# Performance work log

Measured on AMD Instinct MI355X. Metric: run time of the kernel, lower is better.

## Reference

```python
import jax, jax.numpy as jnp
import numpy as np

D = 256          # d_model
NH = 8           # heads
NP = 4           # points per level
NL = 4           # feature levels
DH = D // NH     # head dim = 32
MLP = 4 * D      # 1024
B = 2
SHAPES = [(128, 128), (64, 64), (32, 32), (16, 16)]
LQ = sum(h * w for h, w in SHAPES)  # 21760
EPS = 1e-6


def layer_norm(x, g, b):
    mu = jnp.mean(x, axis=-1, keepdims=True)
    var = jnp.mean(jnp.square(x - mu), axis=-1, keepdims=True)
    return (x - mu) * jax.lax.rsqrt(var + EPS) * g + b


def bilinear_sample(val_l, loc, Hs, Ws):
    # val_l: [B, Hs*Ws, NH, DH]; loc: [B, Lq, NH, NP, 2] normalized in [0,1]
    v = val_l.transpose(0, 2, 1, 3)                      # [B, NH, HW, DH]
    x = loc[..., 0] * Ws - 0.5                           # [B, Lq, NH, NP]
    y = loc[..., 1] * Hs - 0.5
    x0 = jnp.floor(x); y0 = jnp.floor(y)
    lx = x - x0; ly = y - y0
    x0i = x0.astype(jnp.int32); y0i = y0.astype(jnp.int32)

    def gather(xi, yi):
        inb = (xi >= 0) & (xi < Ws) & (yi >= 0) & (yi < Hs)
        idx = jnp.clip(yi, 0, Hs - 1) * Ws + jnp.clip(xi, 0, Ws - 1)
        idx = idx.transpose(0, 2, 1, 3)                  # [B, NH, Lq, NP]
        sh = idx.shape
        idxf = idx.reshape(sh[0], sh[1], -1)
        g = jax.vmap(jax.vmap(lambda vv, ii: vv[ii]))(v, idxf)
        g = g.reshape(sh[0], sh[1], sh[2], sh[3], v.shape[-1])
        return g * inb.transpose(0, 2, 1, 3)[..., None].astype(g.dtype)

    wt = lambda a: a.transpose(0, 2, 1, 3)[..., None]    # -> [B, NH, Lq, NP, 1]
    out = (gather(x0i, y0i) * wt((1 - lx) * (1 - ly))
           + gather(x0i + 1, y0i) * wt(lx * (1 - ly))
           + gather(x0i, y0i + 1) * wt((1 - lx) * ly)
           + gather(x0i + 1, y0i + 1) * wt(lx * ly))
    return out                                            # [B, NH, Lq, NP, DH]


def setup_inputs() -> dict:
    key = jax.random.key(0)
    ks = jax.random.split(key, 16)
    ss = np.array(SHAPES, dtype=np.int64)
    lsi = np.concatenate([[0], np.cumsum(ss[:, 0] * ss[:, 1])[:-1]]).astype(np.int64)
    s = 0.02
    return {
        'src': jax.random.normal(ks[0], (B, LQ, D), jnp.float32),
        'pos': jax.random.normal(ks[1], (B, LQ, D), jnp.float32),
        'reference_points': jax.random.uniform(ks[2], (B, LQ, NL, 2), jnp.float32),
        'spatial_shapes': ss,
        'level_start_index': lsi,
        'g1': jnp.ones((D,), jnp.float32), 'beta1': jnp.zeros((D,), jnp.float32),
        'w_off': jax.random.normal(ks[3], (D, NH * NL * NP * 2), jnp.float32) * 0.01,
        'b_off': jax.random.normal(ks[4], (NH * NL * NP * 2,), jnp.float32) * 0.1,
        'w_attn': jax.random.normal(ks[5], (D, NH * NL * NP), jnp.float32) * s,
        'b_attn': jnp.zeros((NH * NL * NP,), jnp.float32),
        'w_val': jax.random.normal(ks[6], (D, D), jnp.float32) * s,
        'b_val': jnp.zeros((D,), jnp.float32),
        'w_out': jax.random.normal(ks[7], (D, D), jnp.float32) * s,
        'b_out': jnp.zeros((D,), jnp.float32),
        'g2': jnp.ones((D,), jnp.float32), 'beta2': jnp.zeros((D,), jnp.float32),
        'w_fc1': jax.random.normal(ks[8], (D, MLP), jnp.float32) * s,
        'b_fc1': jnp.zeros((MLP,), jnp.float32),
        'w_fc2': jax.random.normal(ks[9], (MLP, D), jnp.float32) * s,
        'b_fc2': jnp.zeros((D,), jnp.float32),
    }


def reference(src, pos, reference_points, spatial_shapes, level_start_index,
              g1, beta1, w_off, b_off, w_attn, b_attn, w_val, b_val,
              w_out, b_out, g2, beta2, w_fc1, b_fc1, w_fc2, b_fc2):
    ss = np.asarray(spatial_shapes)
    lsi = np.asarray(level_start_index)
    Bsz, Lq, _ = src.shape

    # --- pre-norm + multi-scale deformable attention + residual ---
    x = layer_norm(src, g1, beta1)
    q = x + pos
    val = (x @ w_val + b_val).reshape(Bsz, Lq, NH, DH)
    off = (q @ w_off + b_off).reshape(Bsz, Lq, NH, NL, NP, 2)
    aw = jax.nn.softmax((q @ w_attn + b_attn).reshape(Bsz, Lq, NH, NL * NP), axis=-1)
    aw = aw.reshape(Bsz, Lq, NH, NL, NP)

    out = jnp.zeros((Bsz, Lq, NH, DH), src.dtype)
    for l in range(NL):
        Hs, Ws = int(ss[l, 0]), int(ss[l, 1])
        start = int(lsi[l])
        vl = val[:, start:start + Hs * Ws]                       # [B, HW, NH, DH]
        norm = jnp.array([Ws, Hs], src.dtype)
        loc = reference_points[:, :, None, l, None, :] + off[:, :, :, l] / norm
        samp = bilinear_sample(vl, loc, Hs, Ws)                  # [B, NH, Lq, NP, DH]
        a = aw[:, :, :, l].transpose(0, 2, 1, 3)                 # [B, NH, Lq, NP]
        out = out + jnp.einsum('bhqp,bhqpd->bqhd', a, samp)
    attn_out = out.reshape(Bsz, Lq, D) @ w_out + b_out
    src2 = src + attn_out

    # --- pre-norm MLP + residual ---
    y = layer_norm(src2, g2, beta2)
    ffn = jax.nn.relu(y @ w_fc1 + b_fc1) @ w_fc2 + b_fc2
    return src2 + ffn
```

## Files before the change

kernel.cpp:

```cpp
#include <hip/hip_runtime.h>

#define DMODEL 256
#define NHEAD 8
#define NPOINT 4
#define NLEVEL 4
#define DHEAD 32
#define MLPD 1024
#define BSZ 2
#define LQTOK 21760
#define NTOK (BSZ * LQTOK)
#define LNEPS 1e-6f

typedef __attribute__((ext_vector_type(8))) short short8;
typedef __attribute__((ext_vector_type(4))) float f32x4;
typedef __attribute__((ext_vector_type(2))) float f32x2;

__device__ __forceinline__ float bf2f(unsigned short u) {
  unsigned int i = ((unsigned int)u) << 16;
  return __builtin_bit_cast(float, i);
}
__device__ __forceinline__ unsigned short f2bf(float f) {
  unsigned int i = __builtin_bit_cast(unsigned int, f);
  i += 0x7fff + ((i >> 16) & 1);
  return (unsigned short)(i >> 16);
}
__device__ __forceinline__ float bflo(unsigned int u) {
  return __builtin_bit_cast(float, u << 16);
}
__device__ __forceinline__ float bfhi(unsigned int u) {
  return __builtin_bit_cast(float, u & 0xffff0000u);
}

__device__ __forceinline__ void pk_fma_blo(f32x2& d, f32x2 a, f32x2 b) {
  asm("v_pk_fma_f32 %0, %1, %2, %0 op_sel:[0,0,0] op_sel_hi:[1,0,1]"
      : "+v"(d)
      : "v"(a), "v"(b));
}
__device__ __forceinline__ void pk_fma_bhi(f32x2& d, f32x2 a, f32x2 b) {
  asm("v_pk_fma_f32 %0, %1, %2, %0 op_sel:[0,1,0] op_sel_hi:[1,1,1]"
      : "+v"(d)
      : "v"(a), "v"(b));
}

__device__ __forceinline__ void gload_lds16(const unsigned short* g,
                                            unsigned short* lds) {
  __builtin_amdgcn_global_load_lds(
      (const __attribute__((address_space(1))) unsigned int*)g,
      (__attribute__((address_space(3))) unsigned int*)lds, 16, 0, 0);
}

template <bool EMITQ>
__global__ __launch_bounds__(256) void ln_bf16(
    const float* __restrict__ in, const float* __restrict__ g,
    const float* __restrict__ beta, unsigned short* __restrict__ o,
    const float* __restrict__ pos, unsigned short* __restrict__ q) {
  const int w = threadIdx.x >> 6, lane = threadIdx.x & 63;
  const size_t t = (size_t)blockIdx.x * 4 + w;
  const size_t base = t * DMODEL + lane * 4;
  float4 v = *(const float4*)(in + base);
  float s = (v.x + v.y) + (v.z + v.w);
#pragma unroll
  for (int off = 32; off; off >>= 1) s += __shfl_xor(s, off, 64);
  float mu = s * (1.0f / DMODEL);
  float dx = v.x - mu, dy = v.y - mu, dz = v.z - mu, dw = v.w - mu;
  float s2 = (dx * dx + dy * dy) + (dz * dz + dw * dw);
#pragma unroll
  for (int off = 32; off; off >>= 1) s2 += __shfl_xor(s2, off, 64);
  float rs = rsqrtf(s2 * (1.0f / DMODEL) + LNEPS);
  float4 gg = *(const float4*)(g + lane * 4);
  float4 bb = *(const float4*)(beta + lane * 4);
  unsigned short r0 = f2bf(dx * rs * gg.x + bb.x);
  unsigned short r1 = f2bf(dy * rs * gg.y + bb.y);
  unsigned short r2 = f2bf(dz * rs * gg.z + bb.z);
  unsigned short r3 = f2bf(dw * rs * gg.w + bb.w);
  unsigned int lo = ((unsigned int)r1 << 16) | r0;
  unsigned int hi = ((unsigned int)r3 << 16) | r2;
  *(uint2*)(o + base) = make_uint2(lo, hi);
  if (EMITQ) {
    float4 p = *(const float4*)(pos + base);
    unsigned short q0 = f2bf(bf2f(r0) + p.x);
    unsigned short q1 = f2bf(bf2f(r1) + p.y);
    unsigned short q2 = f2bf(bf2f(r2) + p.z);
    unsigned short q3 = f2bf(bf2f(r3) + p.w);
    unsigned int ql = ((unsigned int)q1 << 16) | q0;
    unsigned int qh = ((unsigned int)q3 << 16) | q2;
    *(uint2*)(q + base) = make_uint2(ql, qh);
  }
}

__global__ __launch_bounds__(256) void transpose_bf16(const float* __restrict__ W,
                                                      unsigned short* __restrict__ Wt,
                                                      int K, int N) {
  __shared__ float tile[32][33];
  int k0 = blockIdx.x * 32, n0 = blockIdx.y * 32;
  int tx = threadIdx.x & 31, ty = threadIdx.x >> 5;
  for (int i = ty; i < 32; i += 8) tile[i][tx] = W[(size_t)(k0 + i) * N + n0 + tx];
  __syncthreads();
  for (int i = ty; i < 32; i += 8)
    Wt[(size_t)(n0 + i) * K + k0 + tx] = f2bf(tile[tx][i]);
}

template <int OMODE>
__global__ __launch_bounds__(256) void gemm_mfma(
    const unsigned short* __restrict__ A, const unsigned short* __restrict__ Wt,
    const float* __restrict__ bias, const float* __restrict__ res,
    void* __restrict__ Cout, void* __restrict__ Cout2, int M, int N, int K) {
  __shared__ __attribute__((aligned(16))) unsigned short As[128 * 32];
  __shared__ __attribute__((aligned(16))) unsigned short Bs[128 * 32];
  const int tid = threadIdx.x;
  const unsigned gx = gridDim.x, gy = gridDim.y;
  const unsigned nwg = gx * gy;
  const unsigned orig = blockIdx.y * gx + blockIdx.x;
  const unsigned xcd = orig & 7u, rest = orig >> 3;
  const unsigned qq = nwg >> 3, rr = nwg & 7u;
  const unsigned wgid =
      (xcd < rr ? xcd * (qq + 1) : rr * (qq + 1) + (xcd - rr) * qq) + rest;
  const int m0 = (int)(wgid / gy) * 128;
  const int n0 = (int)(wgid % gy) * 128;
  const int wave = tid >> 6, lane = tid & 63;
  const int wm = (wave & 1) * 64, wn = (wave >> 1) * 64;
  const int lr = lane & 15, quad = lane >> 4;
  f32x4 acc[4][4] = {};
  for (int k0 = 0; k0 < K; k0 += 32) {
    __syncthreads();
#pragma unroll
    for (int r = 0; r < 2; r++) {
      int c = r * 256 + tid;
      int row = c >> 2, col8 = (c & 3) * 8;
      gload_lds16(Wt + (size_t)(n0 + row) * K + k0 + col8,
                  &Bs[(r * 256 + wave * 64) * 8]);
    }
#pragma unroll
    for (int r = 0; r < 2; r++) {
      int c = r * 256 + tid;
      int row = c >> 2, col8 = (c & 3) * 8;
      gload_lds16(A + (size_t)(m0 + row) * K + k0 + col8,
                  &As[(r * 256 + wave * 64) * 8]);
    }
    __syncthreads();
    short8 af[4], bfr[4];
#pragma unroll
    for (int i = 0; i < 4; i++)
      af[i] = *(const short8*)(&As[(wm + i * 16 + lr) * 32 + quad * 8]);
#pragma unroll
    for (int j = 0; j < 4; j++)
      bfr[j] = *(const short8*)(&Bs[(wn + j * 16 + lr) * 32 + quad * 8]);
#pragma unroll
    for (int i = 0; i < 4; i++)
#pragma unroll
      for (int j = 0; j < 4; j++)
        acc[i][j] = __builtin_amdgcn_mfma_f32_16x16x32_bf16(af[i], bfr[j],
                                                            acc[i][j], 0, 0, 0);
  }
#pragma unroll
  for (int i = 0; i < 4; i++) {
    int rbase = m0 + wm + i * 16 + quad * 4;
#pragma unroll
    for (int j = 0; j < 4; j++) {
      int col = n0 + wn + j * 16 + lr;
      float bv = (OMODE == 4 && col >= 256) ? res[col - 256] : bias[col];
#pragma unroll
      for (int r = 0; r < 4; r++) {
        float v = acc[i][j][r] + bv;
        if (OMODE == 2) v = fmaxf(v, 0.0f);
        if (OMODE == 4) {
          size_t row = (size_t)(rbase + r);
          if (col < 256)
            ((unsigned short*)Cout)[row * 256 + col] = f2bf(v);
          else
            ((unsigned short*)Cout2)[row * 128 + (col - 256)] = f2bf(v);
        } else {
          size_t idx = (size_t)(rbase + r) * N + col;
          if (OMODE == 3) {
            ((float*)Cout)[idx] = v + res[idx];
          } else {
            ((unsigned short*)Cout)[idx] = f2bf(v);
          }
        }
      }
    }
  }
}

__global__ __launch_bounds__(256) void deform_sample(
    const unsigned short* __restrict__ val, const unsigned short* __restrict__ off,
    const unsigned short* __restrict__ logits, const float* __restrict__ refp,
    unsigned short* __restrict__ out) {
  __shared__ __attribute__((aligned(16))) int sIdx[4][16][8][4];
  __shared__ __attribute__((aligned(16))) float sW[4][16][8][4];
  const int w = threadIdx.x >> 6, lane = threadIdx.x & 63;
  const int bq = blockIdx.x * 4 + w;
  const int b = __builtin_amdgcn_readfirstlane(bq / LQTOK);
  {
    const int HW_[4] = {128, 64, 32, 16};
    const int LSI_[4] = {0, 16384, 20480, 21504};
    int u0 = 2 * lane;
    int h = u0 >> 4;
    int lvl = (u0 >> 2) & 3;
    int pt0 = u0 & 15;
    int HW = HW_[lvl];
    float2 rp = ((const float2*)refp)[(size_t)bq * 4 + lvl];
    uint2 ov = *(const uint2*)(off + (size_t)bq * 256 + 4 * lane);
    unsigned int lgu = *(const unsigned int*)(logits + (size_t)bq * 128 + 2 * lane);
    float lg0 = bflo(lgu), lg1 = bfhi(lgu);
    float mx = fmaxf(lg0, lg1);
#pragma unroll
    for (int s = 1; s < 8; s <<= 1) mx = fmaxf(mx, __shfl_xor(mx, s, 64));
    float e0 = expf(lg0 - mx), e1 = expf(lg1 - mx);
    float es = e0 + e1;
#pragma unroll
    for (int s = 1; s < 8; s <<= 1) es += __shfl_xor(es, s, 64);
    float inv = 1.0f / es;
    float a01[2] = {e0 * inv, e1 * inv};
    unsigned int ovv[2] = {ov.x, ov.y};
    int hb2 = h * (DHEAD * 2);
#pragma unroll
    for (int c = 0; c < 2; c++) {
      float x = fmaf(rp.x, (float)HW, bflo(ovv[c])) - 0.5f;
      float y = fmaf(rp.y, (float)HW, bfhi(ovv[c])) - 0.5f;
      float xf = floorf(x), yf = floorf(y);
      int x0 = (int)xf, y0 = (int)yf;
      float lx = x - xf, ly = y - yf;
      int x0c = min(max(x0, 0), HW - 1);
      int x1c = min(max(x0 + 1, 0), HW - 1);
      int y0c = min(max(y0, 0), HW - 1);
      int y1c = min(max(y0 + 1, 0), HW - 1);
      float m0x = (x0 >= 0 && x0 < HW) ? 1.f : 0.f;
      float m1x = (x0 + 1 >= 0 && x0 + 1 < HW) ? 1.f : 0.f;
      float m0y = (y0 >= 0 && y0 < HW) ? 1.f : 0.f;
      float m1y = (y0 + 1 >= 0 && y0 + 1 < HW) ? 1.f : 0.f;
      float a = a01[c];
      int pt = pt0 + c;
      int hs = h ^ (pt & 7);
      int r0 = (LSI_[lvl] + y0c * HW) * (DMODEL * 2) + hb2;
      int r1 = (LSI_[lvl] + y1c * HW) * (DMODEL * 2) + hb2;
      *(int4*)sIdx[w][pt][hs] =
          make_int4(r0 + x0c * (DMODEL * 2), r0 + x1c * (DMODEL * 2),
                    r1 + x0c * (DMODEL * 2), r1 + x1c * (DMODEL * 2));
      *(float4*)sW[w][pt][hs] =
          make_float4((1.f - lx) * (1.f - ly) * m0x * m0y * a,
                      lx * (1.f - ly) * m1x * m0y * a,
                      (1.f - lx) * ly * m0x * m1y * a,
                      lx * ly * m1x * m1y * a);
    }
  }
  __builtin_amdgcn_wave_barrier();
  const int h2 = lane >> 3, g = lane & 7;
  const char* basep =
      (const char*)val + (size_t)b * ((size_t)LQTOK * DMODEL * 2);
  const int goff = g * 8;
  f32x2 a01v = {0.f, 0.f}, a23v = {0.f, 0.f};
#pragma unroll
  for (int pb = 0; pb < 4; pb++) {
    int4 ix[4];
    f32x4 wt4[4];
#pragma unroll
    for (int p = 0; p < 4; p++) {
      int pt = pb * 4 + p;
      int hs = h2 ^ (pt & 7);
      ix[p] = *(const int4*)sIdx[w][pt][hs];
      wt4[p] = *(const f32x4*)sW[w][pt][hs];
    }
    uint2 v4[4][4];
#pragma unroll
    for (int p = 0; p < 4; p++) {
      v4[p][0] = *(const uint2*)(basep + (unsigned)(ix[p].x + goff));
      v4[p][1] = *(const uint2*)(basep + (unsigned)(ix[p].y + goff));
      v4[p][2] = *(const uint2*)(basep + (unsigned)(ix[p].z + goff));
      v4[p][3] = *(const uint2*)(basep + (unsigned)(ix[p].w + goff));
    }
#pragma unroll
    for (int p = 0; p < 4; p++) {
      f32x2 w01 = __builtin_shufflevector(wt4[p], wt4[p], 0, 1);
      f32x2 w23 = __builtin_shufflevector(wt4[p], wt4[p], 2, 3);
#pragma unroll
      for (int k = 0; k < 4; k++) {
        uint2 u = v4[p][k];
        f32x2 vlo, vhi;
        vlo[0] = bflo(u.x);
        vlo[1] = bfhi(u.x);
        vhi[0] = bflo(u.y);
        vhi[1] = bfhi(u.y);
        f32x2 wp = (k < 2) ? w01 : w23;
        if ((k & 1) == 0) {
          pk_fma_blo(a01v, vlo, wp);
          pk_fma_blo(a23v, vhi, wp);
        } else {
          pk_fma_bhi(a01v, vlo, wp);
          pk_fma_bhi(a23v, vhi, wp);
        }
      }
    }
  }
  unsigned int o0 = ((unsigned int)f2bf(a01v[1]) << 16) | f2bf(a01v[0]);
  unsigned int o1 = ((unsigned int)f2bf(a23v[1]) << 16) | f2bf(a23v[0]);
  *(uint2*)(out + (size_t)bq * 256 + h2 * 32 + g * 4) = make_uint2(o0, o1);
}

extern "C" void kernel_launch(void* const* d_in, const int* in_sizes, int n_in,
                              void* d_out, int out_size, void* d_ws,
                              size_t ws_size, hipStream_t stream) {
  const float* src    = (const float*)d_in[0];
  const float* pos    = (const float*)d_in[1];
  const float* refp   = (const float*)d_in[2];
  const float* g1     = (const float*)d_in[5];
  const float* beta1  = (const float*)d_in[6];
  const float* w_off  = (const float*)d_in[7];
  const float* b_off  = (const float*)d_in[8];
  const float* w_attn = (const float*)d_in[9];
  const float* b_attn = (const float*)d_in[10];
  const float* w_val  = (const float*)d_in[11];
  const float* b_val  = (const float*)d_in[12];
  const float* w_out  = (const float*)d_in[13];
  const float* b_out  = (const float*)d_in[14];
  const float* g2     = (const float*)d_in[15];
  const float* beta2  = (const float*)d_in[16];
  const float* w_fc1  = (const float*)d_in[17];
  const float* b_fc1  = (const float*)d_in[18];
  const float* w_fc2  = (const float*)d_in[19];
  const float* b_fc2  = (const float*)d_in[20];
  float* out = (float*)d_out;

  const size_t NT = (size_t)NTOK;
  unsigned short* b1 = (unsigned short*)d_ws;
  unsigned short* b2 = b1 + NT * 256;
  unsigned short* b3 = b2 + NT * 256;
  unsigned short* b4 = b3 + NT * 256;
  unsigned short* b5 = b4 + NT * 256;
  unsigned short* wvalT  = b5 + NT * 512;
  unsigned short* woffaT = wvalT + 256 * 256;
  unsigned short* woutT  = woffaT + 384 * 256;
  unsigned short* wfc1T  = woutT + 256 * 256;
  unsigned short* wfc2T  = wfc1T + 1024 * 256;

  unsigned short* qb  = b4;
  unsigned short* lgb = b5;
  unsigned short* yb  = b5;
  unsigned short* hid = b1;

  transpose_bf16<<<dim3(8, 8), 256, 0, stream>>>(w_val, wvalT, 256, 256);
  transpose_bf16<<<dim3(8, 8), 256, 0, stream>>>(w_off, woffaT, 256, 256);
  transpose_bf16<<<dim3(8, 4), 256, 0, stream>>>(w_attn, woffaT + 256 * 256,
                                                 256, 128);
  transpose_bf16<<<dim3(8, 8), 256, 0, stream>>>(w_out, woutT, 256, 256);
  transpose_bf16<<<dim3(8, 32), 256, 0, stream>>>(w_fc1, wfc1T, 256, 1024);
  transpose_bf16<<<dim3(32, 8), 256, 0, stream>>>(w_fc2, wfc2T, 1024, 256);

  const int MT = NTOK / 128;

  ln_bf16<true><<<NTOK / 4, 256, 0, stream>>>(src, g1, beta1, b1, pos, qb);
  gemm_mfma<1><<<dim3(MT, 2), 256, 0, stream>>>(b1, wvalT, b_val, nullptr, b2,
                                                nullptr, NTOK, 256, 256);
  gemm_mfma<4><<<dim3(MT, 3), 256, 0, stream>>>(qb, woffaT, b_off, b_attn, b3,
                                                lgb, NTOK, 384, 256);
  deform_sample<<<NTOK / 4, 256, 0, stream>>>(b2, b3, lgb, refp, b1);
  gemm_mfma<3><<<dim3(MT, 2), 256, 0, stream>>>(b1, woutT, b_out, src, out,
                                                nullptr, NTOK, 256, 256);
  ln_bf16<false><<<NTOK / 4, 256, 0, stream>>>(out, g2, beta2, yb, nullptr,
                                               nullptr);
  gemm_mfma<2><<<dim3(MT, 8), 256, 0, stream>>>(yb, wfc1T, b_fc1, nullptr, hid,
                                                nullptr, NTOK, 1024, 256);
  gemm_mfma<3><<<dim3(MT, 2), 256, 0, stream>>>(hid, wfc2T, b_fc2, out, out,
                                                nullptr, NTOK, 256, 1024);
}
```

Measured before the change: 437.8 us.

## Merge weight transposes, fuse value and offset GEMMs, widen deform blocks

The six weight-transpose launches become one kernel that picks its matrix from the block index. The value projection and the offset/attention-logit projection now run in a single GEMM launch with a 5-wide N grid, so the two independent GEMMs share one wave of workgroups and skip a launch and tail. The deformable sampling kernel moves from 4 to 8 waves per block with larger shared buffers. This cuts launch count and tail effects, but the larger deform blocks may change occupancy.

```diff
diff --git a/kernel.cpp b/kernel.cpp
--- a/kernel.cpp
+++ b/kernel.cpp
@@ -47,6 +47,12 @@
   __builtin_amdgcn_global_load_lds(
       (const __attribute__((address_space(1))) unsigned int*)g,
       (__attribute__((address_space(3))) unsigned int*)lds, 16, 0, 0);
+}
+
+__device__ __forceinline__ unsigned xcd_swz(unsigned orig, unsigned nwg) {
+  unsigned xcd = orig & 7u, rest = orig >> 3;
+  unsigned qq = nwg >> 3, rr = nwg & 7u;
+  return (xcd < rr ? xcd * (qq + 1) : rr * (qq + 1) + (xcd - rr) * qq) + rest;
 }
 
 template <bool EMITQ>
@@ -88,13 +94,36 @@
   }
 }
 
-__global__ __launch_bounds__(256) void transpose_bf16(const float* __restrict__ W,
-                                                      unsigned short* __restrict__ Wt,
-                                                      int K, int N) {
+__global__ __launch_bounds__(256) void transpose_all(
+    const float* __restrict__ w_val, const float* __restrict__ w_off,
+    const float* __restrict__ w_attn, const float* __restrict__ w_out,
+    const float* __restrict__ w_fc1, const float* __restrict__ w_fc2,
+    unsigned short* __restrict__ wvalT, unsigned short* __restrict__ woffaT,
+    unsigned short* __restrict__ woutT, unsigned short* __restrict__ wfc1T,
+    unsigned short* __restrict__ wfc2T) {
   __shared__ float tile[32][33];
-  int k0 = blockIdx.x * 32, n0 = blockIdx.y * 32;
+  int bid = blockIdx.x;
+  const float* W;
+  unsigned short* Wt;
+  int K, N, rel;
+  if (bid < 64) {
+    W = w_val; Wt = wvalT; K = 256; N = 256; rel = bid;
+  } else if (bid < 128) {
+    W = w_off; Wt = woffaT; K = 256; N = 256; rel = bid - 64;
+  } else if (bid < 160) {
+    W = w_attn; Wt = woffaT + 256 * 256; K = 256; N = 128; rel = bid - 128;
+  } else if (bid < 224) {
+    W = w_out; Wt = woutT; K = 256; N = 256; rel = bid - 160;
+  } else if (bid < 480) {
+    W = w_fc1; Wt = wfc1T; K = 256; N = 1024; rel = bid - 224;
+  } else {
+    W = w_fc2; Wt = wfc2T; K = 1024; N = 256; rel = bid - 480;
+  }
+  int ktiles = K >> 5;
+  int k0 = (rel % ktiles) * 32, n0 = (rel / ktiles) * 32;
   int tx = threadIdx.x & 31, ty = threadIdx.x >> 5;
-  for (int i = ty; i < 32; i += 8) tile[i][tx] = W[(size_t)(k0 + i) * N + n0 + tx];
+  for (int i = ty; i < 32; i += 8)
+    tile[i][tx] = W[(size_t)(k0 + i) * N + n0 + tx];
   __syncthreads();
   for (int i = ty; i < 32; i += 8)
     Wt[(size_t)(n0 + i) * K + k0 + tx] = f2bf(tile[tx][i]);
@@ -104,17 +133,13 @@
 __global__ __launch_bounds__(256) void gemm_mfma(
     const unsigned short* __restrict__ A, const unsigned short* __restrict__ Wt,
     const float* __restrict__ bias, const float* __restrict__ res,
-    void* __restrict__ Cout, void* __restrict__ Cout2, int M, int N, int K) {
+    void* __restrict__ Cout, int M, int N, int K) {
   __shared__ __attribute__((aligned(16))) unsigned short As[128 * 32];
   __shared__ __attribute__((aligned(16))) unsigned short Bs[128 * 32];
   const int tid = threadIdx.x;
-  const unsigned gx = gridDim.x, gy = gridDim.y;
-  const unsigned nwg = gx * gy;
-  const unsigned orig = blockIdx.y * gx + blockIdx.x;
-  const unsigned xcd = orig & 7u, rest = orig >> 3;
-  const unsigned qq = nwg >> 3, rr = nwg & 7u;
-  const unsigned wgid =
-      (xcd < rr ? xcd * (qq + 1) : rr * (qq + 1) + (xcd - rr) * qq) + rest;
+  const unsigned gy = gridDim.y;
+  const unsigned wgid = xcd_swz(blockIdx.y * gridDim.x + blockIdx.x,
+                                gridDim.x * gy);
   const int m0 = (int)(wgid / gy) * 128;
   const int n0 = (int)(wgid % gy) * 128;
   const int wave = tid >> 6, lane = tid & 63;
@@ -158,38 +183,108 @@
 #pragma unroll
     for (int j = 0; j < 4; j++) {
       int col = n0 + wn + j * 16 + lr;
-      float bv = (OMODE == 4 && col >= 256) ? res[col - 256] : bias[col];
+      float bv = bias[col];
 #pragma unroll
       for (int r = 0; r < 4; r++) {
+        size_t idx = (size_t)(rbase + r) * N + col;
         float v = acc[i][j][r] + bv;
         if (OMODE == 2) v = fmaxf(v, 0.0f);
-        if (OMODE == 4) {
-          size_t row = (size_t)(rbase + r);
-          if (col < 256)
-            ((unsigned short*)Cout)[row * 256 + col] = f2bf(v);
-          else
-            ((unsigned short*)Cout2)[row * 128 + (col - 256)] = f2bf(v);
+        if (OMODE == 3) {
+          ((float*)Cout)[idx] = v + res[idx];
         } else {
-          size_t idx = (size_t)(rbase + r) * N + col;
-          if (OMODE == 3) {
-            ((float*)Cout)[idx] = v + res[idx];
-          } else {
-            ((unsigned short*)Cout)[idx] = f2bf(v);
-          }
+          ((unsigned short*)Cout)[idx] = f2bf(v);
         }
       }
     }
   }
 }
 
-__global__ __launch_bounds__(256) void deform_sample(
+__global__ __launch_bounds__(256) void gemm_vo(
+    const unsigned short* __restrict__ Ax, const unsigned short* __restrict__ Aq,
+    const unsigned short* __restrict__ Wval,
+    const unsigned short* __restrict__ Woa, const float* __restrict__ bval,
+    const float* __restrict__ boff, const float* __restrict__ battn,
+    unsigned short* __restrict__ oval, unsigned short* __restrict__ ooff,
+    unsigned short* __restrict__ olg) {
+  __shared__ __attribute__((aligned(16))) unsigned short As[128 * 32];
+  __shared__ __attribute__((aligned(16))) unsigned short Bs[128 * 32];
+  const int tid = threadIdx.x;
+  const unsigned gy = gridDim.y;
+  const unsigned wgid = xcd_swz(blockIdx.y * gridDim.x + blockIdx.x,
+                                gridDim.x * gy);
+  const int m0 = (int)(wgid / gy) * 128;
+  const int ny = (int)(wgid % gy);
+  const bool isval = ny < 2;
+  const unsigned short* A = isval ? Ax : Aq;
+  const unsigned short* Wt = isval ? Wval : Woa;
+  const int n0 = isval ? ny * 128 : (ny - 2) * 128;
+  const int wave = tid >> 6, lane = tid & 63;
+  const int wm = (wave & 1) * 64, wn = (wave >> 1) * 64;
+  const int lr = lane & 15, quad = lane >> 4;
+  f32x4 acc[4][4] = {};
+  for (int k0 = 0; k0 < 256; k0 += 32) {
+    __syncthreads();
+#pragma unroll
+    for (int r = 0; r < 2; r++) {
+      int c = r * 256 + tid;
+      int row = c >> 2, col8 = (c & 3) * 8;
+      gload_lds16(Wt + (size_t)(n0 + row) * 256 + k0 + col8,
+                  &Bs[(r * 256 + wave * 64) * 8]);
+    }
+#pragma unroll
+    for (int r = 0; r < 2; r++) {
+      int c = r * 256 + tid;
+      int row = c >> 2, col8 = (c & 3) * 8;
+      gload_lds16(A + (size_t)(m0 + row) * 256 + k0 + col8,
+                  &As[(r * 256 + wave * 64) * 8]);
+    }
+    __syncthreads();
+    short8 af[4], bfr[4];
+#pragma unroll
+    for (int i = 0; i < 4; i++)
+      af[i] = *(const short8*)(&As[(wm + i * 16 + lr) * 32 + quad * 8]);
+#pragma unroll
+    for (int j = 0; j < 4; j++)
+      bfr[j] = *(const short8*)(&Bs[(wn + j * 16 + lr) * 32 + quad * 8]);
+#pragma unroll
+    for (int i = 0; i < 4; i++)
+#pragma unroll
+      for (int j = 0; j < 4; j++)
+        acc[i][j] = __builtin_amdgcn_mfma_f32_16x16x32_bf16(af[i], bfr[j],
+                                                            acc[i][j], 0, 0, 0);
+  }
+#pragma unroll
+  for (int i = 0; i < 4; i++) {
+    int rbase = m0 + wm + i * 16 + quad * 4;
+#pragma unroll
+    for (int j = 0; j < 4; j++) {
+      int col = n0 + wn + j * 16 + lr;
+      float bv = isval ? bval[col]
+                       : (col < 256 ? boff[col] : battn[col - 256]);
+#pragma unroll
+      for (int r = 0; r < 4; r++) {
+        size_t row = (size_t)(rbase + r);
+        float v = acc[i][j][r] + bv;
+        if (isval) {
+          oval[row * 256 + col] = f2bf(v);
+        } else if (col < 256) {
+          ooff[row * 256 + col] = f2bf(v);
+        } else {
+          olg[row * 128 + (col - 256)] = f2bf(v);
+        }
+      }
+    }
+  }
+}
+
+__global__ __launch_bounds__(512) void deform_sample(
     const unsigned short* __restrict__ val, const unsigned short* __restrict__ off,
     const unsigned short* __restrict__ logits, const float* __restrict__ refp,
     unsigned short* __restrict__ out) {
-  __shared__ __attribute__((aligned(16))) int sIdx[4][16][8][4];
-  __shared__ __attribute__((aligned(16))) float sW[4][16][8][4];
+  __shared__ __attribute__((aligned(16))) int sIdx[8][16][8][4];
+  __shared__ __attribute__((aligned(16))) float sW[8][16][8][4];
   const int w = threadIdx.x >> 6, lane = threadIdx.x & 63;
-  const int bq = blockIdx.x * 4 + w;
+  const int bq = blockIdx.x * 8 + w;
   const int b = __builtin_amdgcn_readfirstlane(bq / LQTOK);
   {
     const int HW_[4] = {128, 64, 32, 16};
@@ -338,28 +433,21 @@
   unsigned short* yb  = b5;
   unsigned short* hid = b1;
 
-  transpose_bf16<<<dim3(8, 8), 256, 0, stream>>>(w_val, wvalT, 256, 256);
-  transpose_bf16<<<dim3(8, 8), 256, 0, stream>>>(w_off, woffaT, 256, 256);
-  transpose_bf16<<<dim3(8, 4), 256, 0, stream>>>(w_attn, woffaT + 256 * 256,
-                                                 256, 128);
-  transpose_bf16<<<dim3(8, 8), 256, 0, stream>>>(w_out, woutT, 256, 256);
-  transpose_bf16<<<dim3(8, 32), 256, 0, stream>>>(w_fc1, wfc1T, 256, 1024);
-  transpose_bf16<<<dim3(32, 8), 256, 0, stream>>>(w_fc2, wfc2T, 1024, 256);
-
   const int MT = NTOK / 128;
 
+  transpose_all<<<736, 256, 0, stream>>>(w_val, w_off, w_attn, w_out, w_fc1,
+                                         w_fc2, wvalT, woffaT, woutT, wfc1T,
+                                         wfc2T);
   ln_bf16<true><<<NTOK / 4, 256, 0, stream>>>(src, g1, beta1, b1, pos, qb);
-  gemm_mfma<1><<<dim3(MT, 2), 256, 0, stream>>>(b1, wvalT, b_val, nullptr, b2,
-                                                nullptr, NTOK, 256, 256);
-  gemm_mfma<4><<<dim3(MT, 3), 256, 0, stream>>>(qb, woffaT, b_off, b_attn, b3,
-                                                lgb, NTOK, 384, 256);
-  deform_sample<<<NTOK / 4, 256, 0, stream>>>(b2, b3, lgb, refp, b1);
+  gemm_vo<<<dim3(MT, 5), 256, 0, stream>>>(b1, qb, wvalT, woffaT, b_val, b_off,
+                                           b_attn, b2, b3, lgb);
+  deform_sample<<<NTOK / 8, 512, 0, stream>>>(b2, b3, lgb, refp, b1);
   gemm_mfma<3><<<dim3(MT, 2), 256, 0, stream>>>(b1, woutT, b_out, src, out,
-                                                nullptr, NTOK, 256, 256);
+                                                NTOK, 256, 256);
   ln_bf16<false><<<NTOK / 4, 256, 0, stream>>>(out, g2, beta2, yb, nullptr,
                                                nullptr);
   gemm_mfma<2><<<dim3(MT, 8), 256, 0, stream>>>(yb, wfc1T, b_fc1, nullptr, hid,
-                                                nullptr, NTOK, 1024, 256);
+                                                NTOK, 1024, 256);
   gemm_mfma<3><<<dim3(MT, 2), 256, 0, stream>>>(hid, wfc2T, b_fc2, out, out,
-                                                nullptr, NTOK, 256, 1024);
-}
+                                                NTOK, 256, 1024);
+}
```

After: 415.0 us. 5.2% less time.
